# Kernel tuning notes

Hardware: AMD Instinct MI355X
Metric: run time of the kernel (lower is better)

The kernel has to match this reference:

```python
import jax, jax.numpy as jnp
import numpy as np

B, N, M, H, IN, OUT, NH = 512, 1024, 64, 512, 256, 256, 4
EPS = 1e-8


def setup_inputs() -> dict:
    key = jax.random.key(0)
    ks = jax.random.split(key, 12)
    s = 0.05  # weight scale for numerical stability
    return {
        "in_data": jax.random.normal(ks[0], (B, IN), jnp.float32),
        "memory": jax.random.normal(ks[1], (B, N, M), jnp.float32),
        "prev_reads": jax.random.normal(ks[2], (NH, B, M), jnp.float32),
        "prev_w_r": jnp.zeros((NH, B, N), jnp.float32),
        "prev_w_w": jnp.zeros((NH, B, N), jnp.float32),
        "h0": jnp.zeros((B, H), jnp.float32),
        "c0": jnp.zeros((B, H), jnp.float32),
        "W_ih": jax.random.normal(ks[3], (4 * H, IN + NH * M), jnp.float32) * s,
        "b_ih": jnp.zeros((4 * H,), jnp.float32),
        "W_hh": jax.random.normal(ks[4], (4 * H, H), jnp.float32) * s,
        "b_hh": jnp.zeros((4 * H,), jnp.float32),
        "W_rh": jax.random.normal(ks[5], (NH, M + 6, H), jnp.float32) * s,
        "b_rh": jnp.zeros((NH, M + 6), jnp.float32),
        "W_wh": jax.random.normal(ks[6], (NH, 3 * M + 6, H), jnp.float32) * s,
        "b_wh": jnp.zeros((NH, 3 * M + 6), jnp.float32),
        "W_out": jax.random.normal(ks[7], (OUT, H + NH * M), jnp.float32) * s,
        "b_out": jnp.zeros((OUT,), jnp.float32),
    }


def _address(h, prev_w, mem, W, b):
    # NTM content + location addressing for one head.
    p = h @ W.T + b  # [B, M+6 (+2M for write)]
    k = jnp.tanh(p[:, :M])
    beta = jax.nn.softplus(p[:, M:M + 1])
    g = jax.nn.sigmoid(p[:, M + 1:M + 2])
    sh = jax.nn.softmax(p[:, M + 2:M + 5], axis=-1)  # shifts {-1,0,+1}
    gamma = 1.0 + jax.nn.softplus(p[:, M + 5:M + 6])
    kn = k / (jnp.linalg.norm(k, axis=-1, keepdims=True) + EPS)
    mn = mem / (jnp.linalg.norm(mem, axis=-1, keepdims=True) + EPS)
    wc = jax.nn.softmax(beta * jnp.einsum('bnm,bm->bn', mn, kn), axis=-1)
    wg = g * wc + (1.0 - g) * prev_w
    ws = (sh[:, 0:1] * jnp.roll(wg, 1, axis=-1)
          + sh[:, 1:2] * wg
          + sh[:, 2:3] * jnp.roll(wg, -1, axis=-1))
    wp = ws ** gamma
    w = wp / (jnp.sum(wp, axis=-1, keepdims=True) + EPS)
    return w, p


def reference(in_data, memory, prev_reads, prev_w_r, prev_w_w, h0, c0,
              W_ih, b_ih, W_hh, b_hh, W_rh, b_rh, W_wh, b_wh, W_out, b_out):
    # controller LSTM step on concat(input, prev reads)
    x = jnp.concatenate([in_data, prev_reads.transpose(1, 0, 2).reshape(B, NH * M)], axis=-1)
    gates = x @ W_ih.T + b_ih + h0 @ W_hh.T + b_hh
    i_g, f_g, g_g, o_g = jnp.split(gates, 4, axis=-1)
    c = jax.nn.sigmoid(f_g) * c0 + jax.nn.sigmoid(i_g) * jnp.tanh(g_g)
    h = jax.nn.sigmoid(o_g) * jnp.tanh(c)

    # interleaved read/write heads (read i sees writes of heads < i)
    mem = memory
    reads = []
    for i in range(NH):
        w_r, _ = _address(h, prev_w_r[i], mem, W_rh[i], b_rh[i])
        reads.append(jnp.einsum('bn,bnm->bm', w_r, mem))
        w_w, p = _address(h, prev_w_w[i], mem, W_wh[i], b_wh[i])
        e = jax.nn.sigmoid(p[:, M + 6:2 * M + 6])
        a = jnp.tanh(p[:, 2 * M + 6:3 * M + 6])
        mem = mem * (1.0 - w_w[:, :, None] * e[:, None, :]) + w_w[:, :, None] * a[:, None, :]

    out = jax.nn.sigmoid(
        jnp.concatenate([h] + reads, axis=-1) @ W_out.T + b_out)
    return out
```

## Files before the change

### kernel.cpp

```cpp
#include <hip/hip_runtime.h>
#include <cmath>

#define B_ 512
#define EPS_ 1e-8f

typedef __bf16 bf16x8 __attribute__((ext_vector_type(8)));
typedef float f32x4 __attribute__((ext_vector_type(4)));

__device__ __forceinline__ float sigmoidf_(float x) { return 1.f / (1.f + expf(-x)); }
__device__ __forceinline__ float softplusf_(float x) { return x > 20.f ? x : log1pf(expf(x)); }
__device__ __forceinline__ unsigned f2bf(float x) {
  union { float f; unsigned u; } v; v.f = x;
  unsigned r = v.u + 0x7FFF + ((v.u >> 16) & 1);
  return r >> 16;
}
__device__ __forceinline__ float bfhi2f(unsigned u) { return __uint_as_float(u & 0xffff0000u); }
__device__ __forceinline__ float bflo2f(unsigned u) { return __uint_as_float(u << 16); }
__device__ __forceinline__ unsigned cvtpk(float a, float b) {
  unsigned r;
  asm("v_cvt_pk_bf16_f32 %0, %1, %2" : "=v"(r) : "v"(a), "v"(b));
  return r;
}
__device__ __forceinline__ float rsq_(float x) {
  float r;
  asm("v_rsq_f32 %0, %1" : "=v"(r) : "v"(x));
  return r;
}

__global__ void k_prep(const float* __restrict__ in_data, const float* __restrict__ prev_reads,
                       const float* __restrict__ h0,
                       const float* __restrict__ W_ih, const float* __restrict__ W_hh,
                       const float* __restrict__ b_ih, const float* __restrict__ b_hh,
                       const float* __restrict__ W_rh, const float* __restrict__ W_wh,
                       const float* __restrict__ W_out,
                       const float* __restrict__ b_rh, const float* __restrict__ b_wh,
                       unsigned short* __restrict__ x2b,
                       unsigned short* __restrict__ Wcatb, float* __restrict__ bcat,
                       unsigned short* __restrict__ W2b, unsigned short* __restrict__ Woutb,
                       float* __restrict__ bcat2) {
  const int stride = gridDim.x * blockDim.x;
  const int t0 = blockIdx.x * blockDim.x + threadIdx.x;
  for (int i = t0; i < 512 * 1024; i += stride) {
    const int b = i >> 10, j = i & 1023;
    float v;
    if (j < 256) v = in_data[(size_t)b * 256 + j];
    else if (j < 512) { const int jj = j - 256; v = prev_reads[(size_t)(jj >> 6) * B_ * 64 + (size_t)b * 64 + (jj & 63)]; }
    else v = h0[(size_t)b * 512 + (j - 512)];
    x2b[i] = (unsigned short)f2bf(v);
  }
  for (int i = t0; i < 2048 * 1024; i += stride) {
    const int j = i >> 10, k = i & 1023;
    Wcatb[i] = (unsigned short)f2bf(k < 512 ? W_ih[(size_t)j * 512 + k] : W_hh[(size_t)j * 512 + (k - 512)]);
  }
  for (int i = t0; i < 2048; i += stride) bcat[i] = b_ih[i] + b_hh[i];
  for (int i = t0; i < 143360; i += stride) W2b[i] = (unsigned short)f2bf(W_rh[i]);
  for (int i = t0; i < 405504; i += stride) W2b[143360 + i] = (unsigned short)f2bf(W_wh[i]);
  for (int i = t0; i < 196608; i += stride) Woutb[i] = (unsigned short)f2bf(W_out[i]);
  for (int i = t0; i < 280; i += stride) bcat2[i] = b_rh[i];
  for (int i = t0; i < 792; i += stride) bcat2[280 + i] = b_wh[i];
}

template <bool SIG>
__global__ __launch_bounds__(64) void k_gemm_mfma(const unsigned short* __restrict__ A, int lda,
                                                  const unsigned short* __restrict__ W,
                                                  const float* __restrict__ bias,
                                                  float* __restrict__ C,
                                                  int Nn, int Kk, int ldc) {
  const int l = threadIdx.x;
  const int m0 = blockIdx.y * 32, n0 = blockIdx.x * 32;
  const int lr = l & 15, lk = (l >> 4) * 8;
  f32x4 acc00 = {0.f, 0.f, 0.f, 0.f}, acc01 = acc00, acc10 = acc00, acc11 = acc00;
  const size_t pa0 = (size_t)(m0 + lr) * lda + lk;
  const size_t pa1 = pa0 + (size_t)16 * lda;
  const bool bok0 = (n0 + lr) < Nn, bok1 = (n0 + 16 + lr) < Nn;
  const size_t pb0 = (size_t)(n0 + lr) * Kk + lk;
  const size_t pb1 = pb0 + (size_t)16 * Kk;
#pragma unroll 4
  for (int k0 = 0; k0 < Kk; k0 += 32) {
    bf16x8 a0 = *(const bf16x8*)(A + pa0 + k0);
    bf16x8 a1 = *(const bf16x8*)(A + pa1 + k0);
    bf16x8 b0 = {}, b1 = {};
    if (bok0) b0 = *(const bf16x8*)(W + pb0 + k0);
    if (bok1) b1 = *(const bf16x8*)(W + pb1 + k0);
    acc00 = __builtin_amdgcn_mfma_f32_16x16x32_bf16(a0, b0, acc00, 0, 0, 0);
    acc01 = __builtin_amdgcn_mfma_f32_16x16x32_bf16(a0, b1, acc01, 0, 0, 0);
    acc10 = __builtin_amdgcn_mfma_f32_16x16x32_bf16(a1, b0, acc10, 0, 0, 0);
    acc11 = __builtin_amdgcn_mfma_f32_16x16x32_bf16(a1, b1, acc11, 0, 0, 0);
  }
  const int orow = (l >> 4) * 4;
  f32x4 accs[2][2] = {{acc00, acc01}, {acc10, acc11}};
#pragma unroll
  for (int mi = 0; mi < 2; ++mi) {
#pragma unroll
    for (int nj = 0; nj < 2; ++nj) {
      const int n = n0 + nj * 16 + lr;
      if (n < Nn) {
        const float bv = bias[n];
#pragma unroll
        for (int r = 0; r < 4; ++r) {
          const int m = m0 + mi * 16 + orow + r;
          float v = accs[mi][nj][r] + bv;
          if (SIG) v = 1.f / (1.f + expf(-v));
          C[(size_t)m * ldc + n] = v;
        }
      }
    }
  }
}

__global__ void k_lstm(const float* __restrict__ gates, const float* __restrict__ c0,
                       unsigned short* __restrict__ Aoutb) {
  const int idx = blockIdx.x * blockDim.x + threadIdx.x;
  const int b = idx >> 9, j = idx & 511;
  const float* g = gates + (size_t)b * 2048;
  const float ig = g[j], fg = g[512 + j], gg = g[1024 + j], og = g[1536 + j];
  const float c = sigmoidf_(fg) * c0[idx] + sigmoidf_(ig) * tanhf(gg);
  Aoutb[(size_t)b * 768 + j] = (unsigned short)f2bf(sigmoidf_(og) * tanhf(c));
}

__global__ __launch_bounds__(1024, 4) void k_mega(const float* __restrict__ mem0,
                                                  const float* __restrict__ P,
                                                  const float* __restrict__ prev_w_r,
                                                  const float* __restrict__ prev_w_w,
                                                  unsigned short* __restrict__ Aoutb) {
  const int b = blockIdx.x;
  const int t = threadIdx.x;
  const int l = t & 63;
  const int w = t >> 6;
  const int p = l & 15;
  const int q = l >> 4;

  __shared__ unsigned short smem[65536];
  __shared__ float Ar[1024], Aw[1024];
  __shared__ float nrm_s[1024];
  __shared__ float wpR[1024], wpW[1024];
  __shared__ float racc[16][64];
  __shared__ unsigned short knbs[512];
  __shared__ float parb[8][8];
  __shared__ unsigned ebp[4][32], abp[4][32];
  __shared__ float pb[2][16][2];
  __shared__ float redB[16], redC[16];

  if (w < 8) {
    const int type = w >> 2, head = w & 3;
    const float* pp = P + (size_t)b * 1072 + (type == 0 ? head * 70 : 280 + head * 198);
    const float kv = tanhf(pp[l]);
    float ss = kv * kv;
#pragma unroll
    for (int off = 32; off > 0; off >>= 1) ss += __shfl_xor(ss, off);
    knbs[w * 64 + l] = (unsigned short)f2bf(kv * rsq_(fmaxf(ss, 1e-20f)));
    if (l == 0) {
      parb[w][0] = softplusf_(pp[64]);
      parb[w][1] = sigmoidf_(pp[65]);
      const float s0 = pp[66], s1 = pp[67], s2 = pp[68];
      const float mx = fmaxf(s0, fmaxf(s1, s2));
      const float e0 = expf(s0 - mx), e1 = expf(s1 - mx), e2 = expf(s2 - mx);
      const float inv = 1.f / (e0 + e1 + e2);
      parb[w][2] = e0 * inv; parb[w][3] = e1 * inv; parb[w][4] = e2 * inv;
      parb[w][5] = 1.f + softplusf_(pp[69]);
    }
    if (type == 1 && l < 32) {
      ebp[head][l] = cvtpk(sigmoidf_(pp[70 + 2 * l]), sigmoidf_(pp[70 + 2 * l + 1]));
      abp[head][l] = cvtpk(tanhf(pp[134 + 2 * l]), tanhf(pp[134 + 2 * l + 1]));
    }
  }

  {
    const float4* src = (const float4*)(mem0 + (size_t)b * 65536);
#pragma unroll 4
    for (int k = 0; k < 16; ++k) {
      const int v = k * 1024 + t;
      const float4 f = src[v];
      const int n = v >> 4, ch = v & 15;
      uint2 pk;
      pk.x = cvtpk(f.x, f.y);
      pk.y = cvtpk(f.z, f.w);
      *(uint2*)((char*)smem + n * 128 + (((ch >> 1) ^ (n & 7)) << 4) + ((ch & 1) << 3)) = pk;
    }
  }
  __syncthreads();

  bf16x8 kb0 = {}, kb1 = {};
  if (p < 8) {
    kb0 = *(const bf16x8*)&knbs[p * 64 + q * 8];
    kb1 = *(const bf16x8*)&knbs[p * 64 + 32 + q * 8];
  }

  auto score_pass = [&](int hj) {
#pragma unroll
    for (int tt = 0; tt < 4; ++tt) {
      const int tile = w * 4 + tt;
      const int row = tile * 16 + p;
      const bf16x8 a0 = *(const bf16x8*)((char*)smem + row * 128 + (((q) ^ (row & 7)) << 4));
      const bf16x8 a1 = *(const bf16x8*)((char*)smem + row * 128 + (((q + 4) ^ (row & 7)) << 4));
      f32x4 sacc = {0.f, 0.f, 0.f, 0.f}, gacc = {0.f, 0.f, 0.f, 0.f};
      sacc = __builtin_amdgcn_mfma_f32_16x16x32_bf16(a0, kb0, sacc, 0, 0, 0);
      sacc = __builtin_amdgcn_mfma_f32_16x16x32_bf16(a1, kb1, sacc, 0, 0, 0);
      gacc = __builtin_amdgcn_mfma_f32_16x16x32_bf16(a0, a0, gacc, 0, 0, 0);
      gacc = __builtin_amdgcn_mfma_f32_16x16x32_bf16(a1, a1, gacc, 0, 0, 0);
      if (p == hj)       *(f32x4*)&Ar[tile * 16 + q * 4] = sacc;
      if (p == 4 + hj)   *(f32x4*)&Aw[tile * 16 + q * 4] = sacc;
      if ((p >> 2) == q) nrm_s[tile * 16 + p] = gacc[p & 3];
    }
  };

  score_pass(0);
  __syncthreads();

  const int h = t >> 9;
  const int th = t & 511;
  const int w8 = (t & 511) >> 6;
  float* Abuf = h ? Aw : Ar;
  float* Wbuf = h ? wpW : wpR;

  for (int i = 0; i < 4; ++i) {
    const float beta = parb[h * 4 + i][0], g = parb[h * 4 + i][1];
    const float sh0 = parb[h * 4 + i][2], sh1 = parb[h * 4 + i][3], sh2 = parb[h * 4 + i][4];
    const float gamma = parb[h * 4 + i][5];
    const float* prevw = (h ? prev_w_w : prev_w_r) + ((size_t)i * 512 + b) * 1024;

    const float pv0 = prevw[th];
    const float pv1 = prevw[th + 512];
    float e2_[2];
    float s = 0.f;
#pragma unroll
    for (int k = 0; k < 2; ++k) {
      const int u = th + 512 * k;
      const float z = beta * Abuf[u] * rsq_(fmaxf(nrm_s[u], 1e-20f));
      e2_[k] = __expf(z);
      s += e2_[k];
    }
    Abuf[th] = e2_[0];
    Abuf[th + 512] = e2_[1];
    if (l == 0)  { pb[h][w8][0] = pv0; pb[h][w8 + 8][0] = pv1; }
    if (l == 63) { pb[h][w8][1] = pv0; pb[h][w8 + 8][1] = pv1; }
#pragma unroll
    for (int off = 32; off > 0; off >>= 1) s += __shfl_xor(s, off);
    if (l == 0) redB[w] = s;
    __syncthreads();

    float gsum = 0.f;
#pragma unroll
    for (int j = 0; j < 8; ++j) gsum += redB[h * 8 + j];
    const float gi = g / gsum;
    const float gm = 1.f - g;
    float s2 = 0.f;
#pragma unroll
    for (int k = 0; k < 2; ++k) {
      const int u = th + 512 * k;
      const float wg0 = gi * Abuf[u] + gm * ((k == 0) ? pv0 : pv1);
      float wgm = __shfl_up(wg0, 1);
      float wgp = __shfl_down(wg0, 1);
      if (l == 0) {
        const int um = (u + 1023) & 1023;
        wgm = gi * Abuf[um] + gm * pb[h][um >> 6][1];
      }
      if (l == 63) {
        const int up = (u + 1) & 1023;
        wgp = gi * Abuf[up] + gm * pb[h][up >> 6][0];
      }
      const float ws = sh0 * wgm + sh1 * wg0 + sh2 * wgp;
      const float wp = (ws > 0.f) ? exp2f(gamma * __log2f(ws)) : 0.f;
      Wbuf[u] = wp;
      s2 += wp;
    }
#pragma unroll
    for (int off = 32; off > 0; off >>= 1) s2 += __shfl_xor(s2, off);
    if (l == 0) redC[w] = s2;
    __syncthreads();

    float ir = 0.f, iw = 0.f;
#pragma unroll
    for (int j = 0; j < 8; ++j) { ir += redC[j]; iw += redC[8 + j]; }
    const float inv2r = 1.f / (ir + EPS_);
    const float inv2w = 1.f / (iw + EPS_);

    float e_0 = 0.f, e_1 = 0.f, e_2 = 0.f, e_3 = 0.f;
    float a_0 = 0.f, a_1 = 0.f, a_2 = 0.f, a_3 = 0.f;
    if (i < 3) {
      const unsigned ue0 = ebp[i][p * 2], ue1 = ebp[i][p * 2 + 1];
      const unsigned ua0 = abp[i][p * 2], ua1 = abp[i][p * 2 + 1];
      e_0 = bflo2f(ue0); e_1 = bfhi2f(ue0); e_2 = bflo2f(ue1); e_3 = bfhi2f(ue1);
      a_0 = bflo2f(ua0); a_1 = bfhi2f(ua0); a_2 = bflo2f(ua1); a_3 = bfhi2f(ua1);
    }

    char* const base0 = (char*)smem + (w * 64 + q) * 128 + ((((p >> 1) ^ q) << 4) | ((p & 1) << 3));
    char* const base1 = (char*)smem + (w * 64 + 4 + q) * 128 + ((((p >> 1) ^ (4 + q)) << 4) | ((p & 1) << 3));
    float r[4] = {0.f, 0.f, 0.f, 0.f};
#pragma unroll 2
    for (int it2 = 0; it2 < 8; ++it2) {
      {
        const int row = w * 64 + it2 * 8 + q;
        char* addr = base0 + it2 * 1024;
        uint2 pk = *(uint2*)addr;
        const float v0 = bflo2f(pk.x), v1 = bfhi2f(pk.x);
        const float v2 = bflo2f(pk.y), v3 = bfhi2f(pk.y);
        const float wr = wpR[row] * inv2r;
        r[0] = fmaf(wr, v0, r[0]); r[1] = fmaf(wr, v1, r[1]);
        r[2] = fmaf(wr, v2, r[2]); r[3] = fmaf(wr, v3, r[3]);
        if (i < 3) {
          const float ww = wpW[row] * inv2w;
          pk.x = cvtpk(fmaf(v0, fmaf(-ww, e_0, 1.f), ww * a_0),
                       fmaf(v1, fmaf(-ww, e_1, 1.f), ww * a_1));
          pk.y = cvtpk(fmaf(v2, fmaf(-ww, e_2, 1.f), ww * a_2),
                       fmaf(v3, fmaf(-ww, e_3, 1.f), ww * a_3));
          *(uint2*)addr = pk;
        }
      }
      {
        const int row = w * 64 + it2 * 8 + 4 + q;
        char* addr = base1 + it2 * 1024;
        uint2 pk = *(uint2*)addr;
        const float v0 = bflo2f(pk.x), v1 = bfhi2f(pk.x);
        const float v2 = bflo2f(pk.y), v3 = bfhi2f(pk.y);
        const float wr = wpR[row] * inv2r;
        r[0] = fmaf(wr, v0, r[0]); r[1] = fmaf(wr, v1, r[1]);
        r[2] = fmaf(wr, v2, r[2]); r[3] = fmaf(wr, v3, r[3]);
        if (i < 3) {
          const float ww = wpW[row] * inv2w;
          pk.x = cvtpk(fmaf(v0, fmaf(-ww, e_0, 1.f), ww * a_0),
                       fmaf(v1, fmaf(-ww, e_1, 1.f), ww * a_1));
          pk.y = cvtpk(fmaf(v2, fmaf(-ww, e_2, 1.f), ww * a_2),
                       fmaf(v3, fmaf(-ww, e_3, 1.f), ww * a_3));
          *(uint2*)addr = pk;
        }
      }
    }
#pragma unroll
    for (int c = 0; c < 4; ++c) {
      r[c] += __shfl_xor(r[c], 16);
      r[c] += __shfl_xor(r[c], 32);
    }
    if (q == 0) *(f32x4*)&racc[w][p * 4] = *(f32x4*)r;

    if (i < 3) score_pass(i + 1);
    __syncthreads();

    if (t < 64) {
      float s3 = 0.f;
#pragma unroll
      for (int wv = 0; wv < 16; ++wv) s3 += racc[wv][t];
      Aoutb[(size_t)b * 768 + 512 + i * 64 + t] = (unsigned short)f2bf(s3);
    }
  }
}

extern "C" void kernel_launch(void* const* d_in, const int* in_sizes, int n_in,
                              void* d_out, int out_size, void* d_ws, size_t ws_size,
                              hipStream_t stream) {
  (void)in_sizes; (void)n_in; (void)out_size; (void)ws_size;
  const float* in_data = (const float*)d_in[0];
  const float* memory = (const float*)d_in[1];
  const float* prev_reads = (const float*)d_in[2];
  const float* prev_w_r = (const float*)d_in[3];
  const float* prev_w_w = (const float*)d_in[4];
  const float* h0 = (const float*)d_in[5];
  const float* c0 = (const float*)d_in[6];
  const float* W_ih = (const float*)d_in[7];
  const float* b_ih = (const float*)d_in[8];
  const float* W_hh = (const float*)d_in[9];
  const float* b_hh = (const float*)d_in[10];
  const float* W_rh = (const float*)d_in[11];
  const float* b_rh = (const float*)d_in[12];
  const float* W_wh = (const float*)d_in[13];
  const float* b_wh = (const float*)d_in[14];
  const float* W_out = (const float*)d_in[15];
  const float* b_out = (const float*)d_in[16];
  float* out = (float*)d_out;

  char* base = (char*)d_ws;
  auto alloc = [&](size_t bytes) -> char* {
    char* p = base; base += (bytes + 255) & ~(size_t)255; return p;
  };
  unsigned short* x2b   = (unsigned short*)alloc((size_t)512 * 1024 * 2);
  unsigned short* Wcatb = (unsigned short*)alloc((size_t)2048 * 1024 * 2);
  float* bcat           = (float*)alloc(2048 * 4);
  float* gates          = (float*)alloc((size_t)512 * 2048 * 4);
  unsigned short* W2b   = (unsigned short*)alloc((size_t)1072 * 512 * 2);
  float* bcat2          = (float*)alloc(1072 * 4);
  unsigned short* Woutb = (unsigned short*)alloc((size_t)256 * 768 * 2);
  float* P              = (float*)alloc((size_t)512 * 1072 * 4);
  unsigned short* Aoutb = (unsigned short*)alloc((size_t)512 * 768 * 2);

  k_prep<<<2048, 256, 0, stream>>>(in_data, prev_reads, h0, W_ih, W_hh, b_ih, b_hh,
                                   W_rh, W_wh, W_out, b_rh, b_wh,
                                   x2b, Wcatb, bcat, W2b, Woutb, bcat2);
  k_gemm_mfma<false><<<dim3(64, 16), 64, 0, stream>>>(x2b, 1024, Wcatb, bcat, gates, 2048, 1024, 2048);
  k_lstm<<<1024, 256, 0, stream>>>(gates, c0, Aoutb);
  k_gemm_mfma<false><<<dim3(34, 16), 64, 0, stream>>>(Aoutb, 768, W2b, bcat2, P, 1072, 512, 1072);
  k_mega<<<512, 1024, 0, stream>>>(memory, P, prev_w_r, prev_w_w, Aoutb);
  k_gemm_mfma<true><<<dim3(8, 16), 64, 0, stream>>>(Aoutb, 768, Woutb, b_out, out, 256, 768, 256);
}
```

Baseline: 120.7 us.

## Fuse score softmax-exp into MFMA pass and drop one barrier per head

The MFMA score pass now applies the row-norm scaling, beta and exp in registers, with norms gathered by lane shuffles instead of an nrm_s shared buffer. It also accumulates the softmax partial sums there. The addressing stage no longer has its own exp step and barrier, and the read and write heads are processed by all 1024 threads, one element each. The read normalization is moved after the weighted read reduction, so the per-row multiply in the inner loop disappears. This removes one __syncthreads per head iteration and some shared-memory traffic, at the cost of more work inside the score pass and serial 16-way sums in every thread.

```diff
diff --git a/kernel.cpp b/kernel.cpp
--- a/kernel.cpp
+++ b/kernel.cpp
@@ -132,14 +132,12 @@
 
   __shared__ unsigned short smem[65536];
   __shared__ float Ar[1024], Aw[1024];
-  __shared__ float nrm_s[1024];
   __shared__ float wpR[1024], wpW[1024];
   __shared__ float racc[16][64];
   __shared__ unsigned short knbs[512];
   __shared__ float parb[8][8];
   __shared__ unsigned ebp[4][32], abp[4][32];
-  __shared__ float pb[2][16][2];
-  __shared__ float redB[16], redC[16];
+  __shared__ float redBr[16], redBw[16], redCr[16], redCw[16];
 
   if (w < 8) {
     const int type = w >> 2, head = w & 3;
@@ -186,94 +184,98 @@
     kb1 = *(const bf16x8*)&knbs[p * 64 + 32 + q * 8];
   }
 
-  auto score_pass = [&](int hj) {
+  auto score_exp = [&](int hj) {
+    const float br = parb[hj][0];
+    const float bw = parb[4 + hj][0];
+    const float bsel = (p == hj) ? br : bw;
+    float accR = 0.f, accW = 0.f;
 #pragma unroll
     for (int tt = 0; tt < 4; ++tt) {
       const int tile = w * 4 + tt;
       const int row = tile * 16 + p;
-      const bf16x8 a0 = *(const bf16x8*)((char*)smem + row * 128 + (((q) ^ (row & 7)) << 4));
+      const bf16x8 a0 = *(const bf16x8*)((char*)smem + row * 128 + ((q ^ (row & 7)) << 4));
       const bf16x8 a1 = *(const bf16x8*)((char*)smem + row * 128 + (((q + 4) ^ (row & 7)) << 4));
       f32x4 sacc = {0.f, 0.f, 0.f, 0.f}, gacc = {0.f, 0.f, 0.f, 0.f};
       sacc = __builtin_amdgcn_mfma_f32_16x16x32_bf16(a0, kb0, sacc, 0, 0, 0);
       sacc = __builtin_amdgcn_mfma_f32_16x16x32_bf16(a1, kb1, sacc, 0, 0, 0);
       gacc = __builtin_amdgcn_mfma_f32_16x16x32_bf16(a0, a0, gacc, 0, 0, 0);
       gacc = __builtin_amdgcn_mfma_f32_16x16x32_bf16(a1, a1, gacc, 0, 0, 0);
-      if (p == hj)       *(f32x4*)&Ar[tile * 16 + q * 4] = sacc;
-      if (p == 4 + hj)   *(f32x4*)&Aw[tile * 16 + q * 4] = sacc;
-      if ((p >> 2) == q) nrm_s[tile * 16 + p] = gacc[p & 3];
-    }
+      float nr4[4];
+#pragma unroll
+      for (int r = 0; r < 4; ++r) nr4[r] = __shfl(gacc[r], 20 * q + r);
+      if (p == hj || p == 4 + hj) {
+        f32x4 e4;
+#pragma unroll
+        for (int r = 0; r < 4; ++r)
+          e4[r] = __expf(bsel * sacc[r] * rsq_(fmaxf(nr4[r], 1e-20f)));
+        const float es = e4[0] + e4[1] + e4[2] + e4[3];
+        if (p == hj) { *(f32x4*)&Ar[tile * 16 + q * 4] = e4; accR += es; }
+        else         { *(f32x4*)&Aw[tile * 16 + q * 4] = e4; accW += es; }
+      }
+    }
+    accR += __shfl_xor(accR, 16); accR += __shfl_xor(accR, 32);
+    accW += __shfl_xor(accW, 16); accW += __shfl_xor(accW, 32);
+    if (l == hj)     redBr[w] = accR;
+    if (l == 4 + hj) redBw[w] = accW;
   };
 
-  score_pass(0);
+  score_exp(0);
   __syncthreads();
 
-  const int h = t >> 9;
-  const int th = t & 511;
-  const int w8 = (t & 511) >> 6;
-  float* Abuf = h ? Aw : Ar;
-  float* Wbuf = h ? wpW : wpR;
+  const int u = w * 64 + l;
 
   for (int i = 0; i < 4; ++i) {
-    const float beta = parb[h * 4 + i][0], g = parb[h * 4 + i][1];
-    const float sh0 = parb[h * 4 + i][2], sh1 = parb[h * 4 + i][3], sh2 = parb[h * 4 + i][4];
-    const float gamma = parb[h * 4 + i][5];
-    const float* prevw = (h ? prev_w_w : prev_w_r) + ((size_t)i * 512 + b) * 1024;
-
-    const float pv0 = prevw[th];
-    const float pv1 = prevw[th + 512];
-    float e2_[2];
-    float s = 0.f;
-#pragma unroll
-    for (int k = 0; k < 2; ++k) {
-      const int u = th + 512 * k;
-      const float z = beta * Abuf[u] * rsq_(fmaxf(nrm_s[u], 1e-20f));
-      e2_[k] = __expf(z);
-      s += e2_[k];
-    }
-    Abuf[th] = e2_[0];
-    Abuf[th + 512] = e2_[1];
-    if (l == 0)  { pb[h][w8][0] = pv0; pb[h][w8 + 8][0] = pv1; }
-    if (l == 63) { pb[h][w8][1] = pv0; pb[h][w8 + 8][1] = pv1; }
-#pragma unroll
-    for (int off = 32; off > 0; off >>= 1) s += __shfl_xor(s, off);
-    if (l == 0) redB[w] = s;
+    {
+      float gsum = 0.f;
+#pragma unroll
+      for (int j = 0; j < 16; ++j) gsum += redBr[j];
+      const float g = parb[i][1], sh0 = parb[i][2], sh1 = parb[i][3], sh2 = parb[i][4];
+      const float gamma = parb[i][5];
+      const float gi = g / gsum, gm = 1.f - g;
+      const float* pw = prev_w_r + ((size_t)i * 512 + b) * 1024;
+      const float wg = gi * Ar[u] + gm * pw[u];
+      float wgm = __shfl_up(wg, 1);
+      float wgp = __shfl_down(wg, 1);
+      if (l == 0)  { const int um = (u + 1023) & 1023; wgm = gi * Ar[um] + gm * pw[um]; }
+      if (l == 63) { const int up = (u + 1) & 1023;    wgp = gi * Ar[up] + gm * pw[up]; }
+      const float ws = sh0 * wgm + sh1 * wg + sh2 * wgp;
+      const float wp = (ws > 0.f) ? exp2f(gamma * __log2f(ws)) : 0.f;
+      wpR[u] = wp;
+      float s2 = wp;
+#pragma unroll
+      for (int off = 32; off > 0; off >>= 1) s2 += __shfl_xor(s2, off);
+      if (l == 0) redCr[w] = s2;
+    }
+    if (i < 3) {
+      float gsum = 0.f;
+#pragma unroll
+      for (int j = 0; j < 16; ++j) gsum += redBw[j];
+      const float g = parb[4 + i][1], sh0 = parb[4 + i][2], sh1 = parb[4 + i][3], sh2 = parb[4 + i][4];
+      const float gamma = parb[4 + i][5];
+      const float gi = g / gsum, gm = 1.f - g;
+      const float* pw = prev_w_w + ((size_t)i * 512 + b) * 1024;
+      const float wg = gi * Aw[u] + gm * pw[u];
+      float wgm = __shfl_up(wg, 1);
+      float wgp = __shfl_down(wg, 1);
+      if (l == 0)  { const int um = (u + 1023) & 1023; wgm = gi * Aw[um] + gm * pw[um]; }
+      if (l == 63) { const int up = (u + 1) & 1023;    wgp = gi * Aw[up] + gm * pw[up]; }
+      const float ws = sh0 * wgm + sh1 * wg + sh2 * wgp;
+      const float wp = (ws > 0.f) ? exp2f(gamma * __log2f(ws)) : 0.f;
+      wpW[u] = wp;
+      float s2 = wp;
+#pragma unroll
+      for (int off = 32; off > 0; off >>= 1) s2 += __shfl_xor(s2, off);
+      if (l == 0) redCw[w] = s2;
+    }
     __syncthreads();
 
-    float gsum = 0.f;
-#pragma unroll
-    for (int j = 0; j < 8; ++j) gsum += redB[h * 8 + j];
-    const float gi = g / gsum;
-    const float gm = 1.f - g;
-    float s2 = 0.f;
-#pragma unroll
-    for (int k = 0; k < 2; ++k) {
-      const int u = th + 512 * k;
-      const float wg0 = gi * Abuf[u] + gm * ((k == 0) ? pv0 : pv1);
-      float wgm = __shfl_up(wg0, 1);
-      float wgp = __shfl_down(wg0, 1);
-      if (l == 0) {
-        const int um = (u + 1023) & 1023;
-        wgm = gi * Abuf[um] + gm * pb[h][um >> 6][1];
-      }
-      if (l == 63) {
-        const int up = (u + 1) & 1023;
-        wgp = gi * Abuf[up] + gm * pb[h][up >> 6][0];
-      }
-      const float ws = sh0 * wgm + sh1 * wg0 + sh2 * wgp;
-      const float wp = (ws > 0.f) ? exp2f(gamma * __log2f(ws)) : 0.f;
-      Wbuf[u] = wp;
-      s2 += wp;
-    }
-#pragma unroll
-    for (int off = 32; off > 0; off >>= 1) s2 += __shfl_xor(s2, off);
-    if (l == 0) redC[w] = s2;
-    __syncthreads();
-
-    float ir = 0.f, iw = 0.f;
-#pragma unroll
-    for (int j = 0; j < 8; ++j) { ir += redC[j]; iw += redC[8 + j]; }
-    const float inv2r = 1.f / (ir + EPS_);
-    const float inv2w = 1.f / (iw + EPS_);
+    float inv2w = 0.f;
+    if (i < 3) {
+      float iw = 0.f;
+#pragma unroll
+      for (int j = 0; j < 16; ++j) iw += redCw[j];
+      inv2w = 1.f / (iw + EPS_);
+    }
 
     float e_0 = 0.f, e_1 = 0.f, e_2 = 0.f, e_3 = 0.f;
     float a_0 = 0.f, a_1 = 0.f, a_2 = 0.f, a_3 = 0.f;
@@ -295,7 +297,7 @@
         uint2 pk = *(uint2*)addr;
         const float v0 = bflo2f(pk.x), v1 = bfhi2f(pk.x);
         const float v2 = bflo2f(pk.y), v3 = bfhi2f(pk.y);
-        const float wr = wpR[row] * inv2r;
+        const float wr = wpR[row];
         r[0] = fmaf(wr, v0, r[0]); r[1] = fmaf(wr, v1, r[1]);
         r[2] = fmaf(wr, v2, r[2]); r[3] = fmaf(wr, v3, r[3]);
         if (i < 3) {
@@ -313,7 +315,7 @@
         uint2 pk = *(uint2*)addr;
         const float v0 = bflo2f(pk.x), v1 = bfhi2f(pk.x);
         const float v2 = bflo2f(pk.y), v3 = bfhi2f(pk.y);
-        const float wr = wpR[row] * inv2r;
+        const float wr = wpR[row];
         r[0] = fmaf(wr, v0, r[0]); r[1] = fmaf(wr, v1, r[1]);
         r[2] = fmaf(wr, v2, r[2]); r[3] = fmaf(wr, v3, r[3]);
         if (i < 3) {
@@ -333,14 +335,18 @@
     }
     if (q == 0) *(f32x4*)&racc[w][p * 4] = *(f32x4*)r;
 
-    if (i < 3) score_pass(i + 1);
+    if (i < 3) score_exp(i + 1);
     __syncthreads();
 
     if (t < 64) {
+      float ir = 0.f;
+#pragma unroll
+      for (int j = 0; j < 16; ++j) ir += redCr[j];
+      const float inv2r = 1.f / (ir + EPS_);
       float s3 = 0.f;
 #pragma unroll
       for (int wv = 0; wv < 16; ++wv) s3 += racc[wv][t];
-      Aoutb[(size_t)b * 768 + 512 + i * 64 + t] = (unsigned short)f2bf(s3);
+      Aoutb[(size_t)b * 768 + 512 + i * 64 + t] = (unsigned short)f2bf(s3 * inv2r);
     }
   }
 }
```

After: 126.3 us. 1.05x slower.

## Fold softmax exp and prev-weight load into score pass to drop barrier

Applied to the files above, without the earlier changes.

Each wave now computes the exponentiated content scores for both the read and write heads right after its own score MFMA tiles, and writes per-wave partial sums into separate read and write reduction buffers. It also loads the next head's previous weights before the trailing barrier. This removes one block-wide __syncthreads per head iteration. The final read-vector reduction is deferred to the start of the next iteration, after its barrier. In exchange, the shared-memory hazards rely on each wave only touching its own score rows, and every thread now sums 16 partials instead of 8.

```diff
diff --git a/kernel.cpp b/kernel.cpp
--- a/kernel.cpp
+++ b/kernel.cpp
@@ -139,7 +139,7 @@
   __shared__ float parb[8][8];
   __shared__ unsigned ebp[4][32], abp[4][32];
   __shared__ float pb[2][16][2];
-  __shared__ float redB[16], redC[16];
+  __shared__ float redBr[16], redBw[16], redC[16];
 
   if (w < 8) {
     const int type = w >> 2, head = w & 3;
@@ -204,44 +204,58 @@
     }
   };
 
-  score_pass(0);
-  __syncthreads();
+  auto do_exp = [&](int hj) {
+    const int row = w * 64 + l;
+    const float rn = rsq_(fmaxf(nrm_s[row], 1e-20f));
+    const float per = __expf(parb[hj][0] * Ar[row] * rn);
+    const float pew = __expf(parb[4 + hj][0] * Aw[row] * rn);
+    Ar[row] = per;
+    Aw[row] = pew;
+    float sr = per, sw = pew;
+#pragma unroll
+    for (int off = 32; off > 0; off >>= 1) {
+      sr += __shfl_xor(sr, off);
+      sw += __shfl_xor(sw, off);
+    }
+    if (l == 0) { redBr[w] = sr; redBw[w] = sw; }
+  };
 
   const int h = t >> 9;
   const int th = t & 511;
-  const int w8 = (t & 511) >> 6;
+  const int w8 = th >> 6;
   float* Abuf = h ? Aw : Ar;
   float* Wbuf = h ? wpW : wpR;
 
+  float pv0, pv1;
+  auto load_pw = [&](int ii) {
+    const float* pw = (h ? prev_w_w : prev_w_r) + ((size_t)ii * 512 + b) * 1024;
+    pv0 = pw[th];
+    pv1 = pw[th + 512];
+    if (l == 0)  { pb[h][w8][0] = pv0; pb[h][w8 + 8][0] = pv1; }
+    if (l == 63) { pb[h][w8][1] = pv0; pb[h][w8 + 8][1] = pv1; }
+  };
+
+  score_pass(0);
+  do_exp(0);
+  load_pw(0);
+  __syncthreads();
+
   for (int i = 0; i < 4; ++i) {
-    const float beta = parb[h * 4 + i][0], g = parb[h * 4 + i][1];
+    if (i > 0 && t < 64) {
+      float s3 = 0.f;
+#pragma unroll
+      for (int wv = 0; wv < 16; ++wv) s3 += racc[wv][t];
+      Aoutb[(size_t)b * 768 + 512 + (i - 1) * 64 + t] = (unsigned short)f2bf(s3);
+    }
+    const float g = parb[h * 4 + i][1];
     const float sh0 = parb[h * 4 + i][2], sh1 = parb[h * 4 + i][3], sh2 = parb[h * 4 + i][4];
     const float gamma = parb[h * 4 + i][5];
-    const float* prevw = (h ? prev_w_w : prev_w_r) + ((size_t)i * 512 + b) * 1024;
-
-    const float pv0 = prevw[th];
-    const float pv1 = prevw[th + 512];
-    float e2_[2];
-    float s = 0.f;
-#pragma unroll
-    for (int k = 0; k < 2; ++k) {
-      const int u = th + 512 * k;
-      const float z = beta * Abuf[u] * rsq_(fmaxf(nrm_s[u], 1e-20f));
-      e2_[k] = __expf(z);
-      s += e2_[k];
-    }
-    Abuf[th] = e2_[0];
-    Abuf[th + 512] = e2_[1];
-    if (l == 0)  { pb[h][w8][0] = pv0; pb[h][w8 + 8][0] = pv1; }
-    if (l == 63) { pb[h][w8][1] = pv0; pb[h][w8 + 8][1] = pv1; }
-#pragma unroll
-    for (int off = 32; off > 0; off >>= 1) s += __shfl_xor(s, off);
-    if (l == 0) redB[w] = s;
-    __syncthreads();
-
     float gsum = 0.f;
-#pragma unroll
-    for (int j = 0; j < 8; ++j) gsum += redB[h * 8 + j];
+    {
+      const float* rb = h ? redBw : redBr;
+#pragma unroll
+      for (int j = 0; j < 16; ++j) gsum += rb[j];
+    }
     const float gi = g / gsum;
     const float gm = 1.f - g;
     float s2 = 0.f;
@@ -333,15 +347,19 @@
     }
     if (q == 0) *(f32x4*)&racc[w][p * 4] = *(f32x4*)r;
 
-    if (i < 3) score_pass(i + 1);
+    if (i < 3) {
+      score_pass(i + 1);
+      do_exp(i + 1);
+      load_pw(i + 1);
+    }
     __syncthreads();
-
-    if (t < 64) {
-      float s3 = 0.f;
-#pragma unroll
-      for (int wv = 0; wv < 16; ++wv) s3 += racc[wv][t];
-      Aoutb[(size_t)b * 768 + 512 + i * 64 + t] = (unsigned short)f2bf(s3);
-    }
+  }
+
+  if (t < 64) {
+    float s3 = 0.f;
+#pragma unroll
+    for (int wv = 0; wv < 16; ++wv) s3 += racc[wv][t];
+    Aoutb[(size_t)b * 768 + 512 + 3 * 64 + t] = (unsigned short)f2bf(s3);
   }
 }
 
```

Measured after the change: 124.5 us. 1.03x slower.
